# Kernel optimization log

Measured on AMD Instinct MI355X. Metric: run time of the kernel, lower is better.

Reference implementation:

```python
import jax, jax.numpy as jnp
import numpy as np

SQN = 3      # hardcoded recurrence depth
ATT_H = 256  # hardcoded attention hidden size
STRIDE = 16  # segment length (hardcoded expand(-1,16,-1))


def setup_inputs() -> dict:
    key = jax.random.key(0)
    ks = jax.random.split(key, 12)
    B, Cin, H, V = 64, 512, 512, 512

    def w(k, shape, fan_in):
        return jax.random.normal(k, shape, jnp.float32) / np.sqrt(fan_in).astype(np.float32)

    return {
        "visual_input": jax.random.normal(ks[0], (B, Cin, V), jnp.float32),
        "text_feature": jax.random.normal(ks[1], (B, H), jnp.float32),
        # weights stored [in, out] (transposed vs torch nn.Linear)
        "vis_conv_w": w(ks[2], (Cin, H), Cin),   # 1x1 Conv1d == linear over channels
        "vis_conv_b": jnp.zeros((H,), jnp.float32),
        "glob_w": w(ks[3], (SQN, H, H), H),      # 3 distinct global_emb linears
        "glob_b": jnp.zeros((SQN, H), jnp.float32),
        "guide_w": w(ks[4], (2 * H, H), 2 * H),
        "guide_b": jnp.zeros((H,), jnp.float32),
        "att1_w": w(ks[5], (H, ATT_H), H),
        "att1_b": jnp.zeros((ATT_H,), jnp.float32),
        "att2_w": w(ks[6], (H, ATT_H), H),
        "att2_b": jnp.zeros((ATT_H,), jnp.float32),
        "att3_w": w(ks[7], (ATT_H, 1), ATT_H),
        "att3_b": jnp.zeros((1,), jnp.float32),
        "out_conv_w": w(ks[8], (H, H), H),       # 1x1 Conv1d
        "out_conv_b": jnp.zeros((H,), jnp.float32),
        "text_w": w(ks[9], (H, H), H),
        "text_b": jnp.zeros((H,), jnp.float32),
    }


def reference(visual_input, text_feature, vis_conv_w, vis_conv_b, glob_w, glob_b,
              guide_w, guide_b, att1_w, att1_b, att2_w, att2_b, att3_w, att3_b,
              out_conv_w, out_conv_b, text_w, text_b):
    B, Cin, V = visual_input.shape
    H = vis_conv_w.shape[1]
    S = V // STRIDE  # number of segments

    # vis_conv (1x1) + relu: [B, H, V]
    vis_h = jax.nn.relu(jnp.einsum('bcv,ch->bhv', visual_input, vis_conv_w)
                        + vis_conv_b[None, :, None])
    # split into segments: [B, S, T=16, H]
    vis_seg = vis_h.reshape(B, H, S, STRIDE).transpose(0, 2, 3, 1)
    # AvgPool1d(kernel=stride) == per-segment mean: [B, S, H]
    avg_seg = vis_seg.mean(axis=2)
    # text projection: [B, H]
    text_att = text_feature @ text_w + text_b

    # precompute att_fn2(vis_seg): [B, S, T, ATT_H] (loop-invariant)
    att2_pre = jnp.einsum('bsth,ha->bsta', vis_seg, att2_w) + att2_b

    prev_se = jnp.zeros((B, S, H), vis_seg.dtype)
    se_list, att_list = [], []
    for m in range(SQN):  # fixed 3-step recurrence, distinct weights per step
        v_n = jnp.einsum('bsh,hk->bsk', avg_seg, glob_w[m]) + glob_b[m]
        # guide_emb (Linear+ReLU) followed by an outer relu == single relu
        g_n = jax.nn.relu(jnp.concatenate([v_n, prev_se], axis=-1) @ guide_w + guide_b)
        att = jnp.tanh((g_n @ att1_w + att1_b)[:, :, None, :] + att2_pre)  # [B,S,T,A]
        att = att @ att3_w + att3_b                                        # [B,S,T,1]
        att = jax.nn.softmax(att, axis=2)  # softmax over the 16 frames
        prev_se = jnp.sum(vis_seg * att, axis=2)  # [B, S, H]
        se_list.append(prev_se)
        att_list.append(att)

    vis_for_att = jnp.stack(se_list, axis=2)  # [B, S, 3, H]
    fuse_att = jax.nn.softmax(jnp.einsum('bsmh,bh->bsm', vis_for_att, text_att), axis=2)
    vis_new = jnp.einsum('bsmh,bsm->bsh', vis_for_att, fuse_att)  # [B, S, H]

    # vis_out_conv (1x1) + relu over stacked segments: [B, H, S]
    vis_out = jax.nn.relu(jnp.einsum('bsh,hk->bks', vis_new, out_conv_w)
                          + out_conv_b[None, :, None])
    att_out = jnp.concatenate(att_list, axis=3)  # [B, S, 16, 3]
    return vis_out, att_out
```

## Files before the change

### kernel.cpp

```cpp
#include <hip/hip_runtime.h>

#define B_   64
#define CIN_ 512
#define H_   512
#define V_   512
#define S_   32
#define T_   16
#define A_   256
#define SQN_ 3
#define BS_  2048

typedef float  f32x4  __attribute__((ext_vector_type(4)));
typedef float  f32x2  __attribute__((ext_vector_type(2)));
typedef short  short8 __attribute__((ext_vector_type(8)));
typedef short  short4v __attribute__((ext_vector_type(4)));
typedef unsigned int uint4v __attribute__((ext_vector_type(4)));

__device__ __forceinline__ unsigned short f2bf(float f) {
    union { float f; unsigned int u; } v; v.f = f;
    unsigned int u = v.u;
    unsigned int r = (u + 0x7fffu + ((u >> 16) & 1u)) >> 16;
    return (unsigned short)r;
}
__device__ __forceinline__ float bf2f(unsigned short h) {
    union { unsigned int u; float f; } v; v.u = ((unsigned int)h) << 16;
    return v.f;
}

__device__ __forceinline__ float fast_tanhf(float x) {
    float cx = fminf(fmaxf(x, -15.0f), 15.0f);
    float e  = __expf(2.0f * cx);
    return (e - 1.0f) * __builtin_amdgcn_rcpf(e + 1.0f);
}

__device__ __forceinline__ void gload16(const void* g, void* l) {
    __builtin_amdgcn_global_load_lds(
        (const __attribute__((address_space(1))) unsigned int*)g,
        (__attribute__((address_space(3))) unsigned int*)l,
        16, 0, 0);
}

template <int N> __device__ __forceinline__ void waitv() {
    asm volatile("s_waitcnt vmcnt(%0)" :: "n"(N) : "memory");
}

__global__ __launch_bounds__(256) void prep_kernel(
    const float* __restrict__ visual, const float* __restrict__ vis_conv_w,
    const float* __restrict__ att2_w, const float* __restrict__ guide_w,
    const float* __restrict__ att1_w, const float* __restrict__ out_conv_w,
    const float* __restrict__ glob_w, const float* __restrict__ text_feature,
    const float* __restrict__ text_w, const float* __restrict__ text_b,
    const float* __restrict__ glob_b, const float* __restrict__ guide_b,
    unsigned short* __restrict__ visT, unsigned short* __restrict__ wT_visconv,
    unsigned short* __restrict__ wT_att2, unsigned short* __restrict__ wT_guide,
    unsigned short* __restrict__ wT_att1, unsigned short* __restrict__ wT_out,
    unsigned short* __restrict__ glob_bf, float* __restrict__ text_part,
    float* __restrict__ bcomb)
{
    __shared__ __align__(16) char smem[32768];
    const int id  = blockIdx.x;
    const int tid = threadIdx.x;

    if (id < 128) {
        const int nt = id & 7, kc = id >> 3;
        const int n0 = nt * 64, kbase = kc * 32;
        float* Ts = (float*)smem;
        float* Ws = (float*)smem + 64 * 33;
        {
            const int m = tid >> 2, kk = (tid & 3) * 8;
            #pragma unroll
            for (int c = 0; c < 8; c += 4)
                *(f32x4*)&Ts[m * 33 + kk + c] =
                    *(const f32x4*)&text_feature[m * 512 + kbase + kk + c];
            const int kr = tid >> 3, nn = (tid & 7) * 8;
            #pragma unroll
            for (int c = 0; c < 8; c += 4)
                *(f32x4*)&Ws[kr * 65 + nn + c] =
                    *(const f32x4*)&text_w[(long long)(kbase + kr) * 512 + n0 + nn + c];
        }
        __syncthreads();
        const int tm = (tid >> 4) * 4, tn = (tid & 15) * 4;
        float acc[4][4] = {};
        for (int k = 0; k < 32; k++) {
            float a[4], b2[4];
            #pragma unroll
            for (int i = 0; i < 4; i++) a[i] = Ts[(tm + i) * 33 + k];
            #pragma unroll
            for (int j = 0; j < 4; j++) b2[j] = Ws[k * 65 + tn + j];
            #pragma unroll
            for (int i = 0; i < 4; i++)
                #pragma unroll
                for (int j = 0; j < 4; j++) acc[i][j] += a[i] * b2[j];
        }
        #pragma unroll
        for (int i = 0; i < 4; i++)
            #pragma unroll
            for (int j = 0; j < 4; j++)
                text_part[kc * (64 * 512) + (tm + i) * 512 + n0 + tn + j] =
                    acc[i][j] + (kc == 0 ? text_b[n0 + tn + j] : 0.0f);
        return;
    }
    if (id < 131) {
        const int m = id - 128;
        const int j2 = tid * 2;
        float a0 = guide_b[j2], a1 = guide_b[j2 + 1];
        const float* gb = glob_b + m * 512;
        #pragma unroll 8
        for (int k = 0; k < 512; k++) {
            const float g = gb[k];
            f32x2 w = *(const f32x2*)&guide_w[(long long)k * 512 + j2];
            a0 += g * w[0];
            a1 += g * w[1];
        }
        f32x2 o = {a0, a1};
        *(f32x2*)&bcomb[m * 512 + j2] = o;
        return;
    }
    if (id < 227) {
        const int base = (id - 131) * 8192 + tid * 4;
        #pragma unroll
        for (int it = 0; it < 8; it++) {
            f32x4 v = *(const f32x4*)&glob_w[base + it * 1024];
            short4v o;
            #pragma unroll
            for (int c = 0; c < 4; c++) o[c] = (short)f2bf(v[c]);
            *(short4v*)&glob_bf[base + it * 1024] = o;
        }
        return;
    }

    if (id >= 547) {
        const int q = id - 547;
        const int b = q >> 5, tile = q & 31;
        const int k0 = (tile >> 2) << 6;
        const int v0 = (tile & 3) << 7;
        const float* src = visual + (long long)b * 262144;
        unsigned short* dst = visT + (long long)b * 262144;
        float* tl = (float*)smem;

        const int wave = tid >> 6, lane = tid & 63;
        #pragma unroll
        for (int i = 0; i < 8; i++) {
            const int r2 = wave * 16 + i * 2;
            gload16(&src[(long long)(k0 + r2 + (lane >> 5)) * 512 + v0 + (lane & 31) * 4],
                    &tl[r2 * 128]);
        }
        __syncthreads();

        const int kl = (tid & 7) * 8;
        const int vb = tid >> 3;
        #pragma unroll
        for (int jv = 0; jv < 4; jv++) {
            const int v = vb + jv * 32;
            short8 o;
            #pragma unroll
            for (int i = 0; i < 8; i++)
                o[i] = (short)f2bf(tl[(kl + i) * 128 + v]);
            *(short8*)&dst[(long long)(v0 + v) * 512 + k0 + kl] = o;
        }
        return;
    }

    const float* src; unsigned short* dst; int Kd, Nd, tile;
    if (id < 291)      { tile = id - 227; src = vis_conv_w; dst = wT_visconv; Kd = 512;  Nd = 512; }
    else if (id < 323) { tile = id - 291; src = att2_w;     dst = wT_att2;    Kd = 512;  Nd = 256; }
    else if (id < 451) { tile = id - 323; src = guide_w;    dst = wT_guide;   Kd = 1024; Nd = 512; }
    else if (id < 483) { tile = id - 451; src = att1_w;     dst = wT_att1;    Kd = 512;  Nd = 256; }
    else               { tile = id - 483; src = out_conv_w; dst = wT_out;     Kd = 512;  Nd = 512; }

    unsigned int* tl = (unsigned int*)smem;
    const int xw = Nd >> 6;
    const int n0 = (tile % xw) << 6, k0 = (tile / xw) << 6;
    {
        const int r = tid >> 4;
        const int c4 = (tid & 15) * 4;
        #pragma unroll
        for (int j = 0; j < 4; j++) {
            const int row = j * 16 + r;
            f32x4 v = *(const f32x4*)&src[(long long)(k0 + row) * Nd + n0 + c4];
            #pragma unroll
            for (int c2 = 0; c2 < 4; c2++)
                tl[row * 65 + c4 + c2] = f2bf(v[c2]);
        }
    }
    __syncthreads();
    {
        const int v = tid >> 2, cq = (tid & 3) * 16;
        short8 o0, o1;
        #pragma unroll
        for (int j = 0; j < 8; j++) o0[j] = (short)tl[(cq + j) * 65 + v];
        #pragma unroll
        for (int j = 0; j < 8; j++) o1[j] = (short)tl[(cq + 8 + j) * 65 + v];
        *(short8*)&dst[(long long)(n0 + v) * Kd + k0 + cq] = o0;
        *(short8*)&dst[(long long)(n0 + v) * Kd + k0 + cq + 8] = o1;
    }
}

template <int BM, int BN, bool RELU, bool OUT_BF16, int OUT_MODE, bool ACC_INIT, int DEPTH>
__device__ __forceinline__ void gemm_body(
    char* pool, int bid, int nwg,
    const unsigned short* __restrict__ A, long long aBatch, int lda,
    const unsigned short* __restrict__ Bt, long long bBatch, int ldb,
    const float* __restrict__ bias, long long biasBatch,
    const float* __restrict__ Cinit, int ldci,
    void* __restrict__ C, long long cBatch, int ldc,
    void* __restrict__ C2, unsigned short* __restrict__ avg_out,
    int M, int N, int K)
{
    constexpr int WM = BM / 2, WN = BN / 2;
    constexpr int FI = WM / 16, FJ = WN / 16;
    constexpr int LOADS = BM / 64 + BN / 64;
    constexpr bool CT_EN  = (OUT_MODE != 1);
    constexpr bool CT_F32 = CT_EN && ((OUT_MODE == 0 && !OUT_BF16) || OUT_MODE == 3);
    constexpr int  CTS    = CT_F32 ? (BN + 4) : (BN + 8);
    constexpr int  KLOOP_B = DEPTH * (BM * 32 + BN * 32) * 2;
    constexpr int  CT_B    = CT_EN ? (BM * CTS * (CT_F32 ? 4 : 2)) : 0;
    constexpr int  MAIN_B  = (KLOOP_B > CT_B ? KLOOP_B : CT_B);
    unsigned short* As = (unsigned short*)pool;
    unsigned short* Bs = As + DEPTH * BM * 32;
    float* avgl = (float*)(pool + MAIN_B);

    const int q8 = nwg >> 3, r8 = nwg & 7;
    const int xcd = bid & 7, lid = bid >> 3;
    const int logical = (xcd < r8 ? xcd * (q8 + 1)
                                  : r8 * (q8 + 1) + (xcd - r8) * q8) + lid;

    const int ntiles = N / BN;
    const int tilesPerBatch = (M / BM) * ntiles;
    const int batch = logical / tilesPerBatch;
    const int t     = logical % tilesPerBatch;
    const int tm0 = (t / ntiles) * BM;
    const int tn0 = (t % ntiles) * BN;
    const unsigned short* Ab = A + (long long)batch * aBatch;
    const unsigned short* Bb = Bt + (long long)batch * bBatch;

    const int tid  = threadIdx.x;
    const int lane = tid & 63;
    const int wave = tid >> 6;
    const int wm = (wave >> 1) * WM;
    const int wn = (wave & 1) * WN;
    const int lr = lane & 15;
    const int lk = (lane >> 4) * 8;
    const int rsub = lane >> 2;
    const int g8s = ((lane & 3) ^ ((lane >> 3) & 3)) * 8;
    const int lks = lk ^ (((lr >> 1) & 3) << 3);

    auto stage = [&](int buf, int k0) {
        #pragma unroll
        for (int i = 0; i < BM / 64; i++) {
            const int rbase = wave * (BM / 4) + i * 16;
            gload16(&Ab[(long long)(tm0 + rbase + rsub) * lda + k0 + g8s],
                    &As[buf * (BM * 32) + rbase * 32]);
        }
        #pragma unroll
        for (int i = 0; i < BN / 64; i++) {
            const int rbase = wave * (BN / 4) + i * 16;
            gload16(&Bb[(long long)(tn0 + rbase + rsub) * ldb + k0 + g8s],
                    &Bs[buf * (BN * 32) + rbase * 32]);
        }
    };

    f32x4 acc[FI][FJ] = {};
    const int nk = K >> 5;

    #pragma unroll
    for (int d = 0; d < DEPTH - 1; d++)
        if (d < nk) stage(d, d << 5);

    int cur = 0;
    for (int kt = 0; kt < nk; kt++) {
        if (kt + DEPTH - 1 < nk) {
            const int nb = cur + DEPTH - 1;
            stage(nb >= DEPTH ? nb - DEPTH : nb, (kt + DEPTH - 1) << 5);
        }
        if constexpr (DEPTH == 2) {
            if (kt + 1 < nk) waitv<LOADS>(); else waitv<0>();
        } else {
            if (kt + 2 < nk)      waitv<2 * LOADS>();
            else if (kt + 1 < nk) waitv<LOADS>();
            else                  waitv<0>();
        }
        __builtin_amdgcn_s_barrier();

        const unsigned short* Ac = As + cur * (BM * 32);
        const unsigned short* Bc = Bs + cur * (BN * 32);
        short8 a[FI], b[FJ];
        #pragma unroll
        for (int i = 0; i < FI; i++)
            a[i] = *(const short8*)&Ac[(wm + i * 16 + lr) * 32 + lks];
        #pragma unroll
        for (int j = 0; j < FJ; j++)
            b[j] = *(const short8*)&Bc[(wn + j * 16 + lr) * 32 + lks];
        #pragma unroll
        for (int i = 0; i < FI; i++)
            #pragma unroll
            for (int j = 0; j < FJ; j++)
                acc[i][j] = __builtin_amdgcn_mfma_f32_16x16x32_bf16(
                    a[i], b[j], acc[i][j], 0, 0, 0);
        __builtin_amdgcn_sched_barrier(0);
        __builtin_amdgcn_s_barrier();
        cur = (cur + 1 == DEPTH) ? 0 : cur + 1;
    }

    const int erow = (lane >> 4) * 4;
    const int ecol = lane & 15;

    if constexpr (OUT_MODE == 1) {
        #pragma unroll
        for (int i = 0; i < FI; i++) {
            #pragma unroll
            for (int j = 0; j < FJ; j++) {
                const int gcol = tn0 + wn + j * 16 + ecol;
                const float bv = bias ? bias[gcol] : 0.0f;
                const int grow0 = tm0 + wm + i * 16 + erow;
                const int bb = grow0 >> 5, ss = grow0 & 31;
                f32x4 o;
                #pragma unroll
                for (int r = 0; r < 4; r++) o[r] = fmaxf(acc[i][j][r] + bv, 0.0f);
                *(f32x4*)&((float*)C)[(long long)bb * (H_ * S_) + gcol * S_ + ss] = o;
            }
        }
        return;
    } else {
        __syncthreads();
        unsigned short* CTh = (unsigned short*)pool;
        float*          CTf = (float*)pool;

        #pragma unroll
        for (int i = 0; i < FI; i++) {
            #pragma unroll
            for (int j = 0; j < FJ; j++) {
                const int lcol = wn + j * 16 + ecol;
                const int gcol = tn0 + lcol;
                const float bv = bias ? bias[(long long)batch * biasBatch + gcol] : 0.0f;
                float csum = 0.0f;
                #pragma unroll
                for (int r = 0; r < 4; r++) {
                    const int lrow = wm + i * 16 + erow + r;
                    float v = acc[i][j][r] + bv;
                    if (ACC_INIT) v += Cinit[(long long)(tm0 + lrow) * ldci + gcol];
                    if (RELU) v = fmaxf(v, 0.0f);
                    if constexpr (CT_F32) CTf[lrow * CTS + lcol] = v;
                    else                  CTh[lrow * CTS + lcol] = f2bf(v);
                    if constexpr (OUT_MODE == 2) csum += v;
                }
                if constexpr (OUT_MODE == 2) {
                    csum += __shfl_xor(csum, 16, 64);
                    csum += __shfl_xor(csum, 32, 64);
                    if (lane < 16)
                        avgl[((wm >> 4) + i) * BN + wn + j * 16 + lane] = csum;
                }
            }
        }
        __syncthreads();

        if constexpr (CT_F32) {
            constexpr int ITERS = (BM * BN) / 1024;
            #pragma unroll
            for (int it = 0; it < ITERS; it++) {
                const int flat = it * 1024 + tid * 4;
                const int row = flat / BN, col = flat % BN;
                f32x4 vv = *(const f32x4*)&CTf[row * CTS + col];
                if constexpr (OUT_MODE == 3) {
                    if (batch == 0) {
                        short4v p;
                        #pragma unroll
                        for (int c = 0; c < 4; c++) p[c] = (short)f2bf(fmaxf(vv[c], 0.0f));
                        *(short4v*)&((unsigned short*)C2)[(long long)(tm0 + row) * ldc + tn0 + col] = p;
                    } else {
                        *(f32x4*)&((float*)C)[(long long)(batch - 1) * cBatch +
                                              (long long)(tm0 + row) * ldc + tn0 + col] = vv;
                    }
                } else {
                    *(f32x4*)&((float*)C)[(long long)batch * cBatch +
                                          (long long)(tm0 + row) * ldc + tn0 + col] = vv;
                }
            }
        } else {
            constexpr int ITERS = (BM * BN) / 2048;
            #pragma unroll
            for (int it = 0; it < ITERS; it++) {
                const int flat = it * 2048 + tid * 8;
                const int row = flat / BN, col = flat % BN;
                short8 vv = *(const short8*)&CTh[row * CTS + col];
                *(short8*)&((unsigned short*)C)[(long long)batch * cBatch +
                                                (long long)(tm0 + row) * ldc + tn0 + col] = vv;
            }
        }

        if constexpr (OUT_MODE == 2) {
            const int s = tid >> 5, hq = (tid & 31) * 4;
            short4v pk;
            #pragma unroll
            for (int c = 0; c < 4; c++)
                pk[c] = (short)f2bf(avgl[s * BN + hq + c] * (1.0f / 16.0f));
            *(short4v*)&avg_out[((long long)batch * 32 + (tm0 >> 4) + s) * H_ + tn0 + hq] = pk;
        }
    }
}

template <int BM, int BN, bool RELU, bool OUT_BF16, int OUT_MODE, bool ACC_INIT, int DEPTH>
__global__ __launch_bounds__(256) void mfma_gemm(
    const unsigned short* A, long long aBatch, int lda,
    const unsigned short* Bt, long long bBatch, int ldb,
    const float* bias, long long biasBatch,
    const float* Cinit, int ldci,
    void* C, long long cBatch, int ldc,
    void* C2, unsigned short* avg_out,
    int M, int N, int K)
{
    constexpr bool CT_EN  = (OUT_MODE != 1);
    constexpr bool CT_F32 = CT_EN && ((OUT_MODE == 0 && !OUT_BF16) || OUT_MODE == 3);
    constexpr int  CTS    = CT_F32 ? (BN + 4) : (BN + 8);
    constexpr int  KLOOP_B = DEPTH * (BM * 32 + BN * 32) * 2;
    constexpr int  CT_B    = CT_EN ? (BM * CTS * (CT_F32 ? 4 : 2)) : 0;
    constexpr int  MAIN_B  = (KLOOP_B > CT_B ? KLOOP_B : CT_B);
    constexpr int  AVG_B   = (OUT_MODE == 2) ? (BM / 16) * BN * 4 : 0;
    __shared__ __align__(16) char pool[MAIN_B + AVG_B];
    gemm_body<BM, BN, RELU, OUT_BF16, OUT_MODE, ACC_INIT, DEPTH>(
        pool, blockIdx.x, gridDim.x,
        A, aBatch, lda, Bt, bBatch, ldb, bias, biasBatch, Cinit, ldci,
        C, cBatch, ldc, C2, avg_out, M, N, K);
}

__global__ __launch_bounds__(256) void wcomb_visconv_kernel(
    const unsigned short* wT_guide, const unsigned short* glob_bf,
    unsigned short* WcombT,
    const unsigned short* visT, const unsigned short* wT_visconv,
    const float* vis_conv_b, unsigned short* vis_seg, unsigned short* avg)
{
    __shared__ __align__(16) char pool[38912];
    if (blockIdx.x < 192) {
        gemm_body<64, 64, false, true, 0, false, 2>(pool, blockIdx.x, 192,
            wT_guide, 0, 1024,
            glob_bf, (long long)H_ * H_, H_,
            nullptr, 0, nullptr, 0,
            WcombT, (long long)H_ * H_, H_, nullptr, nullptr, H_, H_, H_);
    } else {
        gemm_body<128, 128, true, true, 2, false, 2>(pool, blockIdx.x - 192, 1024,
            visT, (long long)V_ * CIN_, CIN_,
            wT_visconv, 0, CIN_,
            vis_conv_b, 0, nullptr, 0,
            vis_seg, (long long)V_ * H_, H_, nullptr, avg, V_, H_, CIN_);
    }
}

__global__ __launch_bounds__(256) void att2_p_kernel(
    const unsigned short* vis_seg, const unsigned short* wT_att2,
    const float* att2_b, unsigned short* att2_pre,
    const unsigned short* avg, const unsigned short* WcombT,
    const float* bcomb, float* P, unsigned short* gbuf)
{
    __shared__ __align__(16) char pool[34816];
    if (blockIdx.x < 512) {
        gemm_body<128, 128, false, true, 0, false, 2>(pool, blockIdx.x, 512,
            vis_seg, (long long)V_ * H_, H_,
            wT_att2, 0, H_,
            att2_b, 0, nullptr, 0,
            att2_pre, (long long)V_ * A_, A_, nullptr, nullptr, V_, A_, H_);
    } else {
        gemm_body<64, 64, false, false, 3, false, 2>(pool, blockIdx.x - 512, 768,
            avg, 0, H_,
            WcombT, (long long)H_ * H_, H_,
            bcomb, H_, nullptr, 0,
            P, (long long)BS_ * H_, H_, gbuf, nullptr, BS_, H_, H_);
    }
}

template <bool LAST>
__global__ __launch_bounds__(256) void fused_att_kernel(
    const float* __restrict__ att1,
    const unsigned short* __restrict__ att2_pre,
    const float* __restrict__ att3_w,
    const float* __restrict__ att3_b,
    const unsigned short* __restrict__ vis_seg,
    float* __restrict__ se_m,
    unsigned short* __restrict__ pse,
    float* __restrict__ att_out, int m,
    const float* __restrict__ se_base,
    const float* __restrict__ text_part,
    const float* __restrict__ text_b,
    unsigned short* __restrict__ vis_new)
{
    const int bs = blockIdx.x, tid = threadIdx.x;
    const int wave = tid >> 6, lane = tid & 63;
    __shared__ float logits[T_], wts[T_];
    __shared__ float part[3][512];
    __shared__ float redf[4][3];
    __shared__ float swf[3];
    __shared__ float tsh[512];

    if constexpr (LAST) {
        const int b = bs >> 5;
        for (int h = tid; h < 512; h += 256) {
            float s = text_b[h];
            #pragma unroll
            for (int p = 0; p < 16; p++)
                s += text_part[p * (64 * 512) + b * 512 + h];
            tsh[h] = s;
        }
    }

    f32x4 a1r = *(const f32x4*)&att1[(long long)bs * A_ + lane * 4];
    f32x4 w3r = *(const f32x4*)&att3_w[lane * 4];

    #pragma unroll
    for (int qq = 0; qq < 4; qq++) {
        const int t = wave * 4 + qq;
        short4v ap = *(const short4v*)&att2_pre[(long long)(bs * T_ + t) * A_ + lane * 4];
        float x = 0.f;
        #pragma unroll
        for (int c = 0; c < 4; c++)
            x += fast_tanhf(a1r[c] + bf2f((unsigned short)ap[c])) * w3r[c];
        #pragma unroll
        for (int off = 32; off > 0; off >>= 1) x += __shfl_down(x, off, 64);
        if (lane == 0) logits[t] = x + att3_b[0];
    }
    __syncthreads();
    if (tid == 0) {
        float mx = logits[0];
        #pragma unroll
        for (int t = 1; t < T_; t++) mx = fmaxf(mx, logits[t]);
        float s = 0.f;
        #pragma unroll
        for (int t = 0; t < T_; t++) { float e = expf(logits[t] - mx); wts[t] = e; s += e; }
        float inv = 1.0f / s;
        #pragma unroll
        for (int t = 0; t < T_; t++) wts[t] *= inv;
    }
    __syncthreads();
    if (tid < T_) att_out[bs * (T_ * SQN_) + tid * SQN_ + m] = wts[tid];

    const int slot = tid & 63, quarter = tid >> 6;
    float s[8] = {};
    #pragma unroll
    for (int tt = 0; tt < 4; tt++) {
        const int t = quarter * 4 + tt;
        short8 vv = *(const short8*)&vis_seg[(long long)(bs * T_ + t) * H_ + slot * 8];
        const float w = wts[t];
        #pragma unroll
        for (int c = 0; c < 8; c++) s[c] += bf2f((unsigned short)vv[c]) * w;
    }
    if (quarter) {
        #pragma unroll
        for (int c = 0; c < 8; c++) part[quarter - 1][slot * 8 + c] = s[c];
    }
    __syncthreads();
    if (quarter == 0) {
        #pragma unroll
        for (int c = 0; c < 8; c++)
            s[c] += part[0][slot * 8 + c] + part[1][slot * 8 + c] + part[2][slot * 8 + c];
    }

    if constexpr (!LAST) {
        if (quarter == 0) {
            f32x4 o0 = {s[0], s[1], s[2], s[3]};
            f32x4 o1 = {s[4], s[5], s[6], s[7]};
            *(f32x4*)&se_m[(long long)bs * H_ + slot * 8] = o0;
            *(f32x4*)&se_m[(long long)bs * H_ + slot * 8 + 4] = o1;
            short8 p;
            #pragma unroll
            for (int c = 0; c < 8; c++) p[c] = (short)f2bf(s[c]);
            *(short8*)&pse[(long long)bs * H_ + slot * 8] = p;
        }
    } else {
        const float* se0 = se_base + (long long)bs * H_;
        const float* se1 = se_base + (long long)BS_ * H_ + (long long)bs * H_;

        float p0 = 0.f, p1 = 0.f, p2 = 0.f;
        {
            const int h2 = tid * 2;
            float t0 = tsh[h2], t1 = tsh[h2 + 1];
            p0 = se0[h2] * t0 + se0[h2 + 1] * t1;
            p1 = se1[h2] * t0 + se1[h2 + 1] * t1;
        }
        if (quarter == 0) {
            #pragma unroll
            for (int c = 0; c < 8; c++) p2 += s[c] * tsh[slot * 8 + c];
        }
        #pragma unroll
        for (int off = 32; off > 0; off >>= 1) {
            p0 += __shfl_down(p0, off, 64);
            p1 += __shfl_down(p1, off, 64);
            p2 += __shfl_down(p2, off, 64);
        }
        if (lane == 0) { redf[wave][0] = p0; redf[wave][1] = p1; redf[wave][2] = p2; }
        __syncthreads();
        if (tid == 0) {
            float d0 = redf[0][0] + redf[1][0] + redf[2][0] + redf[3][0];
            float d1 = redf[0][1] + redf[1][1] + redf[2][1] + redf[3][1];
            float d2 = redf[0][2] + redf[1][2] + redf[2][2] + redf[3][2];
            float mx = fmaxf(d0, fmaxf(d1, d2));
            float e0 = expf(d0 - mx), e1 = expf(d1 - mx), e2 = expf(d2 - mx);
            float inv = 1.0f / (e0 + e1 + e2);
            swf[0] = e0 * inv; swf[1] = e1 * inv; swf[2] = e2 * inv;
        }
        __syncthreads();
        if (quarter == 0) {
            const float w0 = swf[0], w1 = swf[1], w2 = swf[2];
            short8 p;
            #pragma unroll
            for (int c = 0; c < 8; c++) {
                const int h = slot * 8 + c;
                p[c] = (short)f2bf(w0 * se0[h] + w1 * se1[h] + w2 * s[c]);
            }
            *(short8*)&vis_new[(long long)bs * H_ + slot * 8] = p;
        }
    }
}

extern "C" void kernel_launch(void* const* d_in, const int* in_sizes, int n_in,
                              void* d_out, int out_size, void* d_ws, size_t ws_size,
                              hipStream_t stream)
{
    const float* visual       = (const float*)d_in[0];
    const float* text_feature = (const float*)d_in[1];
    const float* vis_conv_w   = (const float*)d_in[2];
    const float* vis_conv_b   = (const float*)d_in[3];
    const float* glob_w       = (const float*)d_in[4];
    const float* glob_b       = (const float*)d_in[5];
    const float* guide_w      = (const float*)d_in[6];
    const float* guide_b      = (const float*)d_in[7];
    const float* att1_w       = (const float*)d_in[8];
    const float* att1_b       = (const float*)d_in[9];
    const float* att2_w       = (const float*)d_in[10];
    const float* att2_b       = (const float*)d_in[11];
    const float* att3_w       = (const float*)d_in[12];
    const float* att3_b       = (const float*)d_in[13];
    const float* out_conv_w   = (const float*)d_in[14];
    const float* out_conv_b   = (const float*)d_in[15];
    const float* text_w       = (const float*)d_in[16];
    const float* text_b       = (const float*)d_in[17];
    float* out = (float*)d_out;
    float* att_out = out + (B_ * H_ * S_);

    char* base = (char*)d_ws;
    unsigned short* visT     = (unsigned short*)(base + 0);
    unsigned short* vis_seg  = (unsigned short*)(base + 33554432);
    unsigned short* att2_pre = (unsigned short*)(base + 67108864);
    float*          se       = (float*)(base + 100663296);
    float*          P        = (float*)(base + 113246208);
    unsigned short* pse      = (unsigned short*)(base + 125829120);
    unsigned short* gbuf     = (unsigned short*)(base + 127926272);
    float*          att1buf  = (float*)(base + 130023424);
    unsigned short* avg      = (unsigned short*)(base + 132120576);
    unsigned short* vis_new  = (unsigned short*)(base + 134348800);
    char*           wbase    = base + 136445952;
    unsigned short* wT_visconv = (unsigned short*)(wbase + 0);
    unsigned short* wT_att2    = (unsigned short*)(wbase + 524288);
    unsigned short* wT_guide   = (unsigned short*)(wbase + 786432);
    unsigned short* wT_att1    = (unsigned short*)(wbase + 1835008);
    unsigned short* wT_out     = (unsigned short*)(wbase + 2097152);
    unsigned short* glob_bf    = (unsigned short*)(wbase + 2621440);
    unsigned short* WcombT     = (unsigned short*)(wbase + 4194304);
    float*          bcomb      = (float*)(wbase + 5767168);
    float*          text_part  = (float*)(wbase + 6291456);

    prep_kernel<<<dim3(2595), 256, 0, stream>>>(
        visual, vis_conv_w, att2_w, guide_w, att1_w, out_conv_w, glob_w,
        text_feature, text_w, text_b, glob_b, guide_b,
        visT, wT_visconv, wT_att2, wT_guide, wT_att1, wT_out,
        glob_bf, text_part, bcomb);

    wcomb_visconv_kernel<<<dim3(192 + 1024), 256, 0, stream>>>(
        wT_guide, glob_bf, WcombT,
        visT, wT_visconv, vis_conv_b, vis_seg, avg);

    att2_p_kernel<<<dim3(512 + 768), 256, 0, stream>>>(
        vis_seg, wT_att2, att2_b, att2_pre,
        avg, WcombT, bcomb, P, gbuf);

    for (int m = 0; m < SQN_; m++) {
        if (m > 0) {
            mfma_gemm<64, 64, true, true, 0, true, 3><<<dim3(256), 256, 0, stream>>>(
                pse, 0, H_,
                wT_guide + 512, 0, 1024,
                nullptr, 0, P + (long long)(m - 1) * BS_ * H_, H_,
                gbuf, 0, H_, nullptr, nullptr, BS_, H_, H_);
        }
        mfma_gemm<64, 64, false, false, 0, false, 3><<<dim3(128), 256, 0, stream>>>(
            gbuf, 0, H_,
            wT_att1, 0, H_,
            att1_b, 0, nullptr, 0,
            att1buf, 0, A_, nullptr, nullptr, BS_, A_, H_);
        if (m < SQN_ - 1) {
            fused_att_kernel<false><<<dim3(BS_), 256, 0, stream>>>(
                att1buf, att2_pre, att3_w, att3_b, vis_seg,
                se + (long long)m * BS_ * H_, pse, att_out, m,
                nullptr, nullptr, nullptr, nullptr);
        } else {
            fused_att_kernel<true><<<dim3(BS_), 256, 0, stream>>>(
                att1buf, att2_pre, att3_w, att3_b, vis_seg,
                nullptr, nullptr, att_out, m,
                se, text_part, text_b, vis_new);
        }
    }

    mfma_gemm<64, 64, true, false, 1, false, 3><<<dim3(256), 256, 0, stream>>>(
        vis_new, 0, H_,
        wT_out, 0, H_,
        out_conv_b, 0, nullptr, 0,
        out, 0, 0, nullptr, nullptr, BS_, H_, H_);
}
```

Baseline: 165.9 us.

## Compute two batches per workgroup in vis_conv GEMM to reuse weight tiles

Replaces the generic 128x128 vis_conv GEMM path with a dedicated body in which each workgroup handles the same output tile for two consecutive batches. The weight tile is loaded into LDS once and shared by both batches, which halves weight traffic and the workgroup count (1024 to 512). In exchange, LDS per block grows from about 38KB to 52KB and each block holds two accumulator sets, which raises register pressure and may lower occupancy. The epilogue (bias, relu, bf16 store, segment average) is run once per batch.

```diff
diff --git a/kernel.cpp b/kernel.cpp
--- a/kernel.cpp
+++ b/kernel.cpp
@@ -399,6 +399,140 @@
     }
 }
 
+__device__ __forceinline__ void visconv_pair_body(
+    char* pool, int bid, int nwg,
+    const unsigned short* __restrict__ visT,
+    const unsigned short* __restrict__ Bw,
+    const float* __restrict__ bias,
+    unsigned short* __restrict__ vis_seg,
+    unsigned short* __restrict__ avg_out)
+{
+    unsigned short* As = (unsigned short*)pool;
+    unsigned short* Bs = As + 16384;
+    float* avgl = (float*)(pool + 49152);
+
+    const int logical = (bid & 7) * (nwg >> 3) + (bid >> 3);
+    const int pairIdx = logical >> 4;
+    const int t = logical & 15;
+    const int tm0 = (t >> 2) * 128, tn0 = (t & 3) * 128;
+    const int b0 = pairIdx * 2;
+    const unsigned short* A0 = visT + (long long)b0 * (V_ * CIN_);
+    const unsigned short* A1 = A0 + V_ * CIN_;
+
+    const int tid  = threadIdx.x;
+    const int lane = tid & 63, wave = tid >> 6;
+    const int wm = (wave >> 1) * 64, wn = (wave & 1) * 64;
+    const int lr = lane & 15, lk = (lane >> 4) * 8;
+    const int rsub = lane >> 2;
+    const int g8s = ((lane & 3) ^ ((lane >> 3) & 3)) * 8;
+    const int lks = lk ^ (((lr >> 1) & 3) << 3);
+
+    auto stage = [&](int buf, int k0) {
+        #pragma unroll
+        for (int i = 0; i < 2; i++) {
+            const int rbase = wave * 32 + i * 16;
+            gload16(&A0[(long long)(tm0 + rbase + rsub) * CIN_ + k0 + g8s],
+                    &As[(0 + buf) * 4096 + rbase * 32]);
+            gload16(&A1[(long long)(tm0 + rbase + rsub) * CIN_ + k0 + g8s],
+                    &As[(2 + buf) * 4096 + rbase * 32]);
+            gload16(&Bw[(long long)(tn0 + rbase + rsub) * CIN_ + k0 + g8s],
+                    &Bs[buf * 4096 + rbase * 32]);
+        }
+    };
+
+    f32x4 acc0[4][4] = {}, acc1[4][4] = {};
+
+    stage(0, 0);
+    int cur = 0;
+    for (int kt = 0; kt < 16; kt++) {
+        if (kt + 1 < 16) stage(cur ^ 1, (kt + 1) << 5);
+        if (kt + 1 < 16) waitv<6>(); else waitv<0>();
+        __builtin_amdgcn_s_barrier();
+
+        const unsigned short* Bc = Bs + cur * 4096;
+        short8 b[4];
+        #pragma unroll
+        for (int j = 0; j < 4; j++)
+            b[j] = *(const short8*)&Bc[(wn + j * 16 + lr) * 32 + lks];
+        {
+            const unsigned short* Ac = As + cur * 4096;
+            short8 a[4];
+            #pragma unroll
+            for (int i = 0; i < 4; i++)
+                a[i] = *(const short8*)&Ac[(wm + i * 16 + lr) * 32 + lks];
+            #pragma unroll
+            for (int i = 0; i < 4; i++)
+                #pragma unroll
+                for (int j = 0; j < 4; j++)
+                    acc0[i][j] = __builtin_amdgcn_mfma_f32_16x16x32_bf16(
+                        a[i], b[j], acc0[i][j], 0, 0, 0);
+        }
+        {
+            const unsigned short* Ac = As + (2 + cur) * 4096;
+            short8 a[4];
+            #pragma unroll
+            for (int i = 0; i < 4; i++)
+                a[i] = *(const short8*)&Ac[(wm + i * 16 + lr) * 32 + lks];
+            #pragma unroll
+            for (int i = 0; i < 4; i++)
+                #pragma unroll
+                for (int j = 0; j < 4; j++)
+                    acc1[i][j] = __builtin_amdgcn_mfma_f32_16x16x32_bf16(
+                        a[i], b[j], acc1[i][j], 0, 0, 0);
+        }
+        __builtin_amdgcn_sched_barrier(0);
+        __builtin_amdgcn_s_barrier();
+        cur ^= 1;
+    }
+
+    const int erow = (lane >> 4) * 4;
+    const int ecol = lane & 15;
+    unsigned short* CTh = (unsigned short*)pool;
+
+    auto epil = [&](f32x4 (&acc)[4][4], int b) {
+        #pragma unroll
+        for (int i = 0; i < 4; i++) {
+            #pragma unroll
+            for (int j = 0; j < 4; j++) {
+                const int lcol = wn + j * 16 + ecol;
+                const float bv = bias[tn0 + lcol];
+                float csum = 0.0f;
+                #pragma unroll
+                for (int r = 0; r < 4; r++) {
+                    const int lrow = wm + i * 16 + erow + r;
+                    float v = fmaxf(acc[i][j][r] + bv, 0.0f);
+                    CTh[lrow * 136 + lcol] = f2bf(v);
+                    csum += v;
+                }
+                csum += __shfl_xor(csum, 16, 64);
+                csum += __shfl_xor(csum, 32, 64);
+                if (lane < 16)
+                    avgl[((wm >> 4) + i) * 128 + wn + j * 16 + lane] = csum;
+            }
+        }
+        __syncthreads();
+        #pragma unroll
+        for (int it = 0; it < 8; it++) {
+            const int flat = it * 2048 + tid * 8;
+            const int row = flat >> 7, col = flat & 127;
+            short8 vv = *(const short8*)&CTh[row * 136 + col];
+            *(short8*)&vis_seg[(long long)b * (V_ * H_) +
+                               (long long)(tm0 + row) * H_ + tn0 + col] = vv;
+        }
+        {
+            const int s = tid >> 5, hq = (tid & 31) * 4;
+            short4v pk;
+            #pragma unroll
+            for (int c = 0; c < 4; c++)
+                pk[c] = (short)f2bf(avgl[s * 128 + hq + c] * (1.0f / 16.0f));
+            *(short4v*)&avg_out[((long long)b * 32 + (tm0 >> 4) + s) * H_ + tn0 + hq] = pk;
+        }
+        __syncthreads();
+    };
+    epil(acc0, b0);
+    epil(acc1, b0 + 1);
+}
+
 template <int BM, int BN, bool RELU, bool OUT_BF16, int OUT_MODE, bool ACC_INIT, int DEPTH>
 __global__ __launch_bounds__(256) void mfma_gemm(
     const unsigned short* A, long long aBatch, int lda,
@@ -429,7 +563,7 @@
     const unsigned short* visT, const unsigned short* wT_visconv,
     const float* vis_conv_b, unsigned short* vis_seg, unsigned short* avg)
 {
-    __shared__ __align__(16) char pool[38912];
+    __shared__ __align__(16) char pool[53248];
     if (blockIdx.x < 192) {
         gemm_body<64, 64, false, true, 0, false, 2>(pool, blockIdx.x, 192,
             wT_guide, 0, 1024,
@@ -437,11 +571,8 @@
             nullptr, 0, nullptr, 0,
             WcombT, (long long)H_ * H_, H_, nullptr, nullptr, H_, H_, H_);
     } else {
-        gemm_body<128, 128, true, true, 2, false, 2>(pool, blockIdx.x - 192, 1024,
-            visT, (long long)V_ * CIN_, CIN_,
-            wT_visconv, 0, CIN_,
-            vis_conv_b, 0, nullptr, 0,
-            vis_seg, (long long)V_ * H_, H_, nullptr, avg, V_, H_, CIN_);
+        visconv_pair_body(pool, blockIdx.x - 192, 512,
+            visT, wT_visconv, vis_conv_b, vis_seg, avg);
     }
 }
 
@@ -662,7 +793,7 @@
         visT, wT_visconv, wT_att2, wT_guide, wT_att1, wT_out,
         glob_bf, text_part, bcomb);
 
-    wcomb_visconv_kernel<<<dim3(192 + 1024), 256, 0, stream>>>(
+    wcomb_visconv_kernel<<<dim3(192 + 512), 256, 0, stream>>>(
         wT_guide, glob_bf, WcombT,
         visT, wT_visconv, vis_conv_b, vis_seg, avg);
 
```

Measured after the change: 164.8 us. Within noise of the previous version (-0.7%).
